# Performance work log

Hardware: AMD Instinct MI355X
Metric: run time of the kernel (lower is better)

## Reference

```python
import jax, jax.numpy as jnp
import numpy as np
from jax import lax

B, CIN, H, W = 8, 256, 128, 128
CC, COUT = 16, 64
KH, KW = 5, 5
PT, PB = KH // 2, (KH + 1) // 2 - 1  # top/bottom pad (SAME-style)
PL, PR = KW // 2, (KW + 1) // 2 - 1


def setup_inputs() -> dict:
    key = jax.random.key(0)
    k1, k2, k3, k4 = jax.random.split(key, 4)
    x = jax.random.normal(k1, (B, CIN, H, W), dtype=jnp.float32)
    W_ext = jax.random.normal(k2, (CC, CIN, 3, 3), dtype=jnp.float32) * 0.05
    b_ext = jax.random.normal(k3, (CC,), dtype=jnp.float32) * 0.05
    W_reg = jax.random.normal(k4, (COUT, CC, KH, KW), dtype=jnp.float32) * 0.05
    return {"x": x, "W_ext": W_ext, "b_ext": b_ext, "W_reg": W_reg}


def reference(x, W_ext, b_ext, W_reg):
    # extract_input: Conv2d(in->corr_channels, 3x3, pad=1)
    f = lax.conv_general_dilated(
        x, W_ext, window_strides=(1, 1), padding=[(1, 1), (1, 1)],
        dimension_numbers=("NCHW", "OIHW", "NCHW"))
    f = f + b_ext[None, :, None, None]  # (B, CC, H, W)

    # Local autocorrelation: corr[b,c,h,w,di,dj] = f[b,c,h,w] * f_pad[b,c,h+di,w+dj]
    fp = jnp.pad(f, ((0, 0), (0, 0), (PT, PB), (PL, PR)))
    # stack shifted views over the fixed kh*kw offsets (small constant loop)
    patches = jnp.stack(
        [fp[:, :, i:i + H, j:j + W] for i in range(KH) for j in range(KW)],
        axis=-1)  # (B, CC, H, W, KH*KW)
    corr = f[..., None] * patches  # (B, CC, H, W, KH*KW) cost volume

    vec = jnp.einsum("bchwk,ock->bohw", corr, W_reg.reshape(COUT, CC, KH * KW))
    return vec  # (B, COUT, H, W)
```

## Files before the change

kernel.cpp:

```cpp
#include <hip/hip_runtime.h>

#define B_    8
#define CIN_  256
#define H_    128
#define W_    128
#define CC_   16
#define COUT_ 64
#define HFP_  132

typedef _Float16 half8 __attribute__((ext_vector_type(8)));
typedef float float4v __attribute__((ext_vector_type(4)));

__global__ void repack_w1(const float* __restrict__ Wext, _Float16* __restrict__ Wa1) {
    int i = blockIdx.x * 256 + threadIdx.x;
    if (i >= 9 * 8 * 64 * 8) return;
    int j    = i & 7;
    int lane = (i >> 3) & 63;
    int blk  = (i >> 9) & 7;
    int tap  = i >> 12;
    int cc   = lane & 15;
    int cin  = blk * 32 + (lane >> 4) * 8 + j;
    Wa1[i] = (_Float16)Wext[cc * (CIN_ * 9) + cin * 9 + tap];
}

__global__ void repack_w2(const float* __restrict__ Wreg, _Float16* __restrict__ Wa2) {
    int u = blockIdx.x * 256 + threadIdx.x;
    if (u >= 4 * 13 * 64 * 8) return;
    int j    = u & 7;
    int lane = (u >> 3) & 63;
    int su   = u >> 9;
    int s    = su % 13;
    int g    = su / 13;
    int q    = lane >> 4;
    int kk   = 2 * s + (q >> 1);
    int c    = (q & 1) * 8 + j;
    int o    = g * 16 + (lane & 15);
    float v  = (kk < 25) ? Wreg[o * (CC_ * 25) + c * 25 + kk] : 0.0f;
    Wa2[u] = (_Float16)v;
}

__global__ __launch_bounds__(256, 2) void conv_fused(
    const float* __restrict__ x, const _Float16* __restrict__ Wa1,
    const float* __restrict__ bext, _Float16* __restrict__ fpad)
{
    __shared__ _Float16 xs[4 * 3170];
    __shared__ _Float16 lt[4][64][16];

    const int lane = threadIdx.x;
    const int wv   = threadIdx.y;
    const int tid  = wv * 64 + lane;
    const int n    = lane & 15;
    const int q    = lane >> 4;
    const int h0   = blockIdx.y * 4;
    const int w0   = blockIdx.x * 64;
    const int b    = blockIdx.z;

    int  goff[7];
    int  loff[7];
    bool vld[7];
#pragma unroll
    for (int p = 0; p < 7; ++p) {
        int u = p * 256 + tid;
        if (u > 1583) u = 0;
        const int col  = u % 66;
        const int pair = u / 66;
        const int row  = pair % 6;
        const int c8   = pair / 6;
        const int hh = h0 - 1 + row;
        const int ww = w0 - 1 + col;
        vld[p] = (hh >= 0) && (hh < H_) && (ww >= 0) && (ww < W_);
        const int hc = hh < 0 ? 0 : (hh > H_ - 1 ? H_ - 1 : hh);
        const int wc = ww < 0 ? 0 : (ww > W_ - 1 ? W_ - 1 : ww);
        goff[p] = (c8 * 8) * (H_ * W_) + hc * W_ + wc;
        loff[p] = c8 * 3170 + (row * 66 + col) * 8;
    }

    const float* xb = x + (size_t)b * (CIN_ * H_ * W_);
    float4v acc[4] = {};

    for (int chunk = 0; chunk < 8; ++chunk) {
        __syncthreads();
        const float* xc = xb + (size_t)chunk * (32 * H_ * W_);
#pragma unroll
        for (int p = 0; p < 7; ++p) {
            if (p != 6 || tid < 48) {
                half8 hv;
#pragma unroll
                for (int j = 0; j < 8; ++j) {
                    const float v = xc[goff[p] + j * (H_ * W_)];
                    hv[j] = (_Float16)(vld[p] ? v : 0.0f);
                }
                *(half8*)(xs + loff[p]) = hv;
            }
        }
        __syncthreads();

        const _Float16* wchunk = Wa1 + (size_t)chunk * 512 + lane * 8;
        const _Float16* xsb    = xs + q * 3170 + (wv * 66 + n) * 8;
#pragma unroll
        for (int r = 0; r < 3; ++r) {
#pragma unroll
            for (int s = 0; s < 3; ++s) {
                const half8 af = *(const half8*)(wchunk + (r * 3 + s) * 4096);
#pragma unroll
                for (int st = 0; st < 4; ++st) {
                    const half8 bf = *(const half8*)(xsb + (r * 66 + s + st * 16) * 8);
                    acc[st] = __builtin_amdgcn_mfma_f32_16x16x32_f16(af, bf, acc[st], 0, 0, 0);
                }
            }
        }
    }

    float bias[4];
#pragma unroll
    for (int rr = 0; rr < 4; ++rr) bias[rr] = bext[q * 4 + rr];

#pragma unroll
    for (int st = 0; st < 4; ++st) {
#pragma unroll
        for (int rr = 0; rr < 4; ++rr) {
            lt[wv][st * 16 + n][q * 4 + rr] = (_Float16)(acc[st][rr] + bias[rr]);
        }
    }
    __syncthreads();

    const half8 o0 = *(const half8*)&lt[wv][lane][0];
    const half8 o1 = *(const half8*)&lt[wv][lane][8];
    _Float16* dst = fpad + (((size_t)b * HFP_ + (h0 + wv + 2)) * HFP_ + (w0 + lane + 2)) * 16;
    *(half8*)dst = o0;
    *(half8*)(dst + 8) = o1;
}

__global__ __launch_bounds__(256, 4) void corr_mfma(
    const _Float16* __restrict__ fpad, const _Float16* __restrict__ Wa2,
    float* __restrict__ out)
{
    const int lane = threadIdx.x;
    const int wv   = threadIdx.y;
    const int n    = lane & 15;
    const int q    = lane >> 4;
    const int h    = blockIdx.y;
    const int w0   = blockIdx.x * 64 + wv * 16;
    const int b    = blockIdx.z;

    const _Float16* fb = fpad + ((size_t)b * HFP_ + h) * (HFP_ * 16);
    const int coff = (q & 1) * 8;

    const half8 ctr = *(const half8*)(fb + (size_t)(2 * HFP_ + (w0 + n + 2)) * 16 + coff);

    float4v acc[4] = {};

#pragma unroll
    for (int s = 0; s < 13; ++s) {
        int kk = 2 * s + (q >> 1);
        if (kk > 24) kk = 24;
        const int ki = kk / 5, kj = kk % 5;
        const half8 sh = *(const half8*)(fb + (size_t)(ki * HFP_ + (w0 + n + kj)) * 16 + coff);
        const half8 corr = ctr * sh;
#pragma unroll
        for (int g = 0; g < 4; ++g) {
            const half8 wf = *(const half8*)(Wa2 + ((size_t)(g * 13 + s) * 64 + lane) * 8);
            acc[g] = __builtin_amdgcn_mfma_f32_16x16x32_f16(wf, corr, acc[g], 0, 0, 0);
        }
    }

#pragma unroll
    for (int g = 0; g < 4; ++g) {
#pragma unroll
        for (int rr = 0; rr < 4; ++rr) {
            const int o = g * 16 + q * 4 + rr;
            out[((size_t)(b * COUT_ + o) * H_ + h) * W_ + (w0 + n)] = acc[g][rr];
        }
    }
}

extern "C" void kernel_launch(void* const* d_in, const int* in_sizes, int n_in,
                              void* d_out, int out_size, void* d_ws, size_t ws_size,
                              hipStream_t stream) {
    const float* x    = (const float*)d_in[0];
    const float* Wext = (const float*)d_in[1];
    const float* bext = (const float*)d_in[2];
    const float* Wreg = (const float*)d_in[3];
    float* out = (float*)d_out;

    char* ws = (char*)d_ws;
    _Float16* fpad = (_Float16*)ws;
    _Float16* Wa1  = (_Float16*)(ws + 4460544);
    _Float16* Wa2  = (_Float16*)(ws + 4460544 + 73728);

    repack_w1<<<dim3(144), dim3(256), 0, stream>>>(Wext, Wa1);
    repack_w2<<<dim3(104), dim3(256), 0, stream>>>(Wreg, Wa2);
    hipMemsetAsync(fpad, 0, (size_t)B_ * CC_ * HFP_ * HFP_ * sizeof(_Float16), stream);

    conv_fused<<<dim3(2, 32, 8), dim3(64, 4), 0, stream>>>(x, Wa1, bext, fpad);
    corr_mfma<<<dim3(2, 128, 8), dim3(64, 4), 0, stream>>>(fpad, Wa2, out);
}
```

Before: 274.2 us.

## Double-buffer input staging in conv and halve tile width for more blocks

The 3x3 conv kernel now prefetches the next 32-channel chunk of x into registers while running MFMAs on the current chunk, then writes it into a second shared-memory buffer. This overlaps global loads with compute. The tile width drops from 64 to 32 columns, doubling the grid and raising the launch-bounds occupancy target. In exchange the halo overhead per tile grows (34/32 vs 66/64 columns) and prefetch registers add pressure.

```diff
diff --git a/kernel.cpp b/kernel.cpp
--- a/kernel.cpp
+++ b/kernel.cpp
@@ -7,6 +7,10 @@
 #define CC_   16
 #define COUT_ 64
 #define HFP_  132
+#define HW_   (H_ * W_)
+
+#define XS_STRIDE 1634
+#define XS_BUF    (4 * XS_STRIDE)
 
 typedef _Float16 half8 __attribute__((ext_vector_type(8)));
 typedef float float4v __attribute__((ext_vector_type(4)));
@@ -39,12 +43,12 @@
     Wa2[u] = (_Float16)v;
 }
 
-__global__ __launch_bounds__(256, 2) void conv_fused(
+__global__ __launch_bounds__(256, 4) void conv_fused(
     const float* __restrict__ x, const _Float16* __restrict__ Wa1,
     const float* __restrict__ bext, _Float16* __restrict__ fpad)
 {
-    __shared__ _Float16 xs[4 * 3170];
-    __shared__ _Float16 lt[4][64][16];
+    __shared__ _Float16 xs[2 * XS_BUF];
+    __shared__ _Float16 lt[4][32][16];
 
     const int lane = threadIdx.x;
     const int wv   = threadIdx.y;
@@ -52,18 +56,20 @@
     const int n    = lane & 15;
     const int q    = lane >> 4;
     const int h0   = blockIdx.y * 4;
-    const int w0   = blockIdx.x * 64;
+    const int w0   = blockIdx.x * 32;
     const int b    = blockIdx.z;
 
-    int  goff[7];
-    int  loff[7];
-    bool vld[7];
-#pragma unroll
-    for (int p = 0; p < 7; ++p) {
+    int  goff[4];
+    int  loff[4];
+    bool vld[4];
+    bool act[4];
+#pragma unroll
+    for (int p = 0; p < 4; ++p) {
         int u = p * 256 + tid;
-        if (u > 1583) u = 0;
-        const int col  = u % 66;
-        const int pair = u / 66;
+        act[p] = (u < 816);
+        if (!act[p]) u = 0;
+        const int col  = u % 34;
+        const int pair = u / 34;
         const int row  = pair % 6;
         const int c8   = pair / 6;
         const int hh = h0 - 1 + row;
@@ -71,44 +77,71 @@
         vld[p] = (hh >= 0) && (hh < H_) && (ww >= 0) && (ww < W_);
         const int hc = hh < 0 ? 0 : (hh > H_ - 1 ? H_ - 1 : hh);
         const int wc = ww < 0 ? 0 : (ww > W_ - 1 ? W_ - 1 : ww);
-        goff[p] = (c8 * 8) * (H_ * W_) + hc * W_ + wc;
-        loff[p] = c8 * 3170 + (row * 66 + col) * 8;
-    }
-
-    const float* xb = x + (size_t)b * (CIN_ * H_ * W_);
-    float4v acc[4] = {};
-
+        goff[p] = (c8 * 8) * HW_ + hc * W_ + wc;
+        loff[p] = c8 * XS_STRIDE + (row * 34 + col) * 8;
+    }
+
+    const float* xb = x + (size_t)b * (CIN_ * HW_);
+    float4v acc[2] = {};
+
+#pragma unroll
+    for (int p = 0; p < 4; ++p) {
+        if (act[p]) {
+            half8 hv;
+#pragma unroll
+            for (int j = 0; j < 8; ++j) {
+                const float v = xb[goff[p] + j * HW_];
+                hv[j] = (_Float16)(vld[p] ? v : 0.0f);
+            }
+            *(half8*)(xs + loff[p]) = hv;
+        }
+    }
+
+    float pf[4][8];
     for (int chunk = 0; chunk < 8; ++chunk) {
         __syncthreads();
-        const float* xc = xb + (size_t)chunk * (32 * H_ * W_);
-#pragma unroll
-        for (int p = 0; p < 7; ++p) {
-            if (p != 6 || tid < 48) {
-                half8 hv;
-#pragma unroll
-                for (int j = 0; j < 8; ++j) {
-                    const float v = xc[goff[p] + j * (H_ * W_)];
-                    hv[j] = (_Float16)(vld[p] ? v : 0.0f);
+        const int cur = chunk & 1;
+
+        if (chunk < 7) {
+            const float* xc = xb + (size_t)(chunk + 1) * (32 * HW_);
+#pragma unroll
+            for (int p = 0; p < 4; ++p) {
+                if (act[p]) {
+#pragma unroll
+                    for (int j = 0; j < 8; ++j)
+                        pf[p][j] = xc[goff[p] + j * HW_];
                 }
-                *(half8*)(xs + loff[p]) = hv;
-            }
-        }
-        __syncthreads();
+            }
+        }
 
         const _Float16* wchunk = Wa1 + (size_t)chunk * 512 + lane * 8;
-        const _Float16* xsb    = xs + q * 3170 + (wv * 66 + n) * 8;
+        const _Float16* xsb    = xs + cur * XS_BUF + q * XS_STRIDE + (wv * 34 + n) * 8;
 #pragma unroll
         for (int r = 0; r < 3; ++r) {
 #pragma unroll
             for (int s = 0; s < 3; ++s) {
                 const half8 af = *(const half8*)(wchunk + (r * 3 + s) * 4096);
 #pragma unroll
-                for (int st = 0; st < 4; ++st) {
-                    const half8 bf = *(const half8*)(xsb + (r * 66 + s + st * 16) * 8);
+                for (int st = 0; st < 2; ++st) {
+                    const half8 bf = *(const half8*)(xsb + (r * 34 + s + st * 16) * 8);
                     acc[st] = __builtin_amdgcn_mfma_f32_16x16x32_f16(af, bf, acc[st], 0, 0, 0);
                 }
             }
         }
+
+        if (chunk < 7) {
+            _Float16* xd = xs + (cur ^ 1) * XS_BUF;
+#pragma unroll
+            for (int p = 0; p < 4; ++p) {
+                if (act[p]) {
+                    half8 hv;
+#pragma unroll
+                    for (int j = 0; j < 8; ++j)
+                        hv[j] = (_Float16)(vld[p] ? pf[p][j] : 0.0f);
+                    *(half8*)(xd + loff[p]) = hv;
+                }
+            }
+        }
     }
 
     float bias[4];
@@ -116,7 +149,7 @@
     for (int rr = 0; rr < 4; ++rr) bias[rr] = bext[q * 4 + rr];
 
 #pragma unroll
-    for (int st = 0; st < 4; ++st) {
+    for (int st = 0; st < 2; ++st) {
 #pragma unroll
         for (int rr = 0; rr < 4; ++rr) {
             lt[wv][st * 16 + n][q * 4 + rr] = (_Float16)(acc[st][rr] + bias[rr]);
@@ -124,11 +157,10 @@
     }
     __syncthreads();
 
-    const half8 o0 = *(const half8*)&lt[wv][lane][0];
-    const half8 o1 = *(const half8*)&lt[wv][lane][8];
-    _Float16* dst = fpad + (((size_t)b * HFP_ + (h0 + wv + 2)) * HFP_ + (w0 + lane + 2)) * 16;
-    *(half8*)dst = o0;
-    *(half8*)(dst + 8) = o1;
+    const half8 o = *(const half8*)&lt[wv][lane >> 1][(lane & 1) * 8];
+    _Float16* dst = fpad + (((size_t)b * HFP_ + (h0 + wv + 2)) * HFP_ + (w0 + (lane >> 1) + 2)) * 16
+                    + (lane & 1) * 8;
+    *(half8*)dst = o;
 }
 
 __global__ __launch_bounds__(256, 4) void corr_mfma(
@@ -192,6 +224,6 @@
     repack_w2<<<dim3(104), dim3(256), 0, stream>>>(Wreg, Wa2);
     hipMemsetAsync(fpad, 0, (size_t)B_ * CC_ * HFP_ * HFP_ * sizeof(_Float16), stream);
 
-    conv_fused<<<dim3(2, 32, 8), dim3(64, 4), 0, stream>>>(x, Wa1, bext, fpad);
+    conv_fused<<<dim3(4, 32, 8), dim3(64, 4), 0, stream>>>(x, Wa1, bext, fpad);
     corr_mfma<<<dim3(2, 128, 8), dim3(64, 4), 0, stream>>>(fpad, Wa2, out);
 }
```

After: 274.2 us. About the same (-0.0%).
